# Performance work log

Hardware: AMD Instinct MI355X
Metric: run time of the kernel (lower is better)

The kernel has to match this reference:

```python
import jax, jax.numpy as jnp
import numpy as np

DN = ('NCDHW', 'OIDHW', 'NCDHW')

def conv(x, w, stride=1):
    k = w.shape[-1]
    pad = 'VALID' if k == 2 else 'SAME'  # ks=2,s=2 Minkowski offsets {0,1}; ks=3 centered; ks=1 pointwise
    return jax.lax.conv_general_dilated(x, w, (stride,) * 3, pad, dimension_numbers=DN)

def masked_bn(x, m, eps=1e-5):
    # BatchNorm over occupied voxels only (MinkowskiBatchNorm semantics); affine is identity at init.
    cnt = jnp.maximum(jnp.sum(m), 1.0)
    mean = jnp.sum(x * m, axis=(0, 2, 3, 4)) / cnt
    xc = (x - mean.reshape(1, -1, 1, 1, 1)) * m  # also zeroes unoccupied sites
    var = jnp.sum(xc * xc, axis=(0, 2, 3, 4)) / cnt
    return xc * jax.lax.rsqrt(var + eps).reshape(1, -1, 1, 1, 1)

def downmask(m):
    B, _, D, H, W = m.shape
    return m.reshape(B, 1, D // 2, 2, H // 2, 2, W // 2, 2).max(axis=(3, 5, 7))

def cbr(x, m, w):
    return jax.nn.relu(masked_bn(conv(x, w), m))

def res(x, m, wa, wb, wsk):
    y = masked_bn(conv(jax.nn.relu(masked_bn(conv(x, wa), m)), wb), m)
    sk = x if wsk is None else masked_bn(conv(x, wsk), m)
    return jax.nn.relu(y + sk)

def stage(x, m, wd, wa1, wb1, wsk, wa2, wb2):
    m2 = downmask(m)  # output coord set of ks=2,s=2 sparse conv
    x = jax.nn.relu(masked_bn(conv(x, wd, 2), m2))  # BasicConvolutionBlock
    x = res(x, m2, wa1, wb1, wsk)
    x = res(x, m2, wa2, wb2, None)
    return x, m2

def _forward(feats, mask, ws0, ws1, d1, a11, b11, a12, b12, d2, a21, b21, k2, a22, b22,
             d3, a31, b31, k3, a32, b32, d4, a41, b41, k4, a42, b42):
    m = mask
    x = cbr(feats * m, m, ws0)
    x = cbr(x, m, ws1)
    x, m = stage(x, m, d1, a11, b11, None, a12, b12)   # 32 -> 32 (identity skip)
    x, m = stage(x, m, d2, a21, b21, k2, a22, b22)     # 32 -> 64
    x, m = stage(x, m, d3, a31, b31, k3, a32, b32)     # 64 -> 128
    x, m = stage(x, m, d4, a41, b41, k4, a42, b42)     # 128 -> 256
    return x

def setup_inputs() -> dict:
    key = jax.random.key(0)
    ks = jax.random.split(key, 28)
    def W(k, o, i, s):
        return jax.random.normal(k, (o, i, s, s, s), jnp.float32) / np.sqrt(i * s ** 3)
    feats = jax.random.normal(ks[0], (2, 3, 64, 64, 64), jnp.float32)
    mask = (jax.random.uniform(ks[1], (2, 1, 64, 64, 64)) < 0.1).astype(jnp.float32)
    return dict(
        feats=feats * mask, mask=mask,
        ws0=W(ks[2], 32, 3, 3), ws1=W(ks[3], 32, 32, 3),
        d1=W(ks[4], 32, 32, 2), a11=W(ks[5], 32, 32, 3), b11=W(ks[6], 32, 32, 3),
        a12=W(ks[7], 32, 32, 3), b12=W(ks[8], 32, 32, 3),
        d2=W(ks[9], 32, 32, 2), a21=W(ks[10], 64, 32, 3), b21=W(ks[11], 64, 64, 3),
        k2=W(ks[12], 64, 32, 1), a22=W(ks[13], 64, 64, 3), b22=W(ks[14], 64, 64, 3),
        d3=W(ks[15], 64, 64, 2), a31=W(ks[16], 128, 64, 3), b31=W(ks[17], 128, 128, 3),
        k3=W(ks[18], 128, 64, 1), a32=W(ks[19], 128, 128, 3), b32=W(ks[20], 128, 128, 3),
        d4=W(ks[21], 128, 128, 2), a41=W(ks[22], 256, 128, 3), b41=W(ks[23], 256, 256, 3),
        k4=W(ks[24], 256, 128, 1), a42=W(ks[25], 256, 256, 3), b42=W(ks[26], 256, 256, 3))

def reference(feats, mask, ws0, ws1, d1, a11, b11, a12, b12, d2, a21, b21, k2, a22, b22,
              d3, a31, b31, k3, a32, b32, d4, a41, b41, k4, a42, b42):
    return _forward(feats, mask, ws0, ws1, d1, a11, b11, a12, b12, d2, a21, b21, k2, a22, b22,
                    d3, a31, b31, k3, a32, b32, d4, a41, b41, k4, a42, b42)
```

## Files before the change

### kernel.cpp

```cpp
#include <hip/hip_runtime.h>

#define BLK 256

static inline int gup(long work) { return (int)((work + BLK - 1) / BLK); }

__device__ inline bool occ_pred(const float* mask, const int* fmap,
                                int i, int DHW, int Ho, int Wo, int mode) {
  if (mode == 0) return mask[i] > 0.f;
  int b = i / DHW, sp = i - b * DHW;
  int HW = Ho * Wo;
  int z = sp / HW, r = sp - z * HW, y = r / Wo, x = r - y * Wo;
  int Hi = 2 * Ho, Wi = 2 * Wo;
  const int* mb = fmap + b * 8 * DHW;
  int base = ((2 * z) * Hi + 2 * y) * Wi + 2 * x;
  bool occ = false;
  for (int dz = 0; dz < 2; dz++)
    for (int dy = 0; dy < 2; dy++)
      for (int dx = 0; dx < 2; dx++)
        occ |= mb[base + dz * Hi * Wi + dy * Wi + dx] >= 0;
  return occ;
}

__global__ __launch_bounds__(1024) void cnt_k(const float* mask, const int* fmap,
    int* bcnt, int DHW, int Ho, int Wo, int mode, int total) {
  int i = blockIdx.x * 1024 + threadIdx.x;
  bool occ = (i < total) && occ_pred(mask, fmap, i, DHW, Ho, Wo, mode);
  unsigned long long bal = __ballot(occ);
  __shared__ int ws[16];
  int lane = threadIdx.x & 63, wid = threadIdx.x >> 6;
  if (lane == 0) ws[wid] = __popcll(bal);
  __syncthreads();
  if (threadIdx.x == 0) {
    int a = 0;
    for (int w = 0; w < 16; w++) a += ws[w];
    bcnt[blockIdx.x] = a;
  }
}

__global__ __launch_bounds__(1024) void scan_k(int* bcnt, int nb, int* cnt) {
  __shared__ int sh[1024];
  int t = threadIdx.x;
  int v = (t < nb) ? bcnt[t] : 0;
  sh[t] = v;
  __syncthreads();
  for (int o = 1; o < 1024; o <<= 1) {
    int u = (t >= o) ? sh[t - o] : 0;
    __syncthreads();
    sh[t] += u;
    __syncthreads();
  }
  if (t < nb) bcnt[t] = sh[t] - v;
  if (t == 0) *cnt = sh[1023];
}

__global__ __launch_bounds__(1024) void emit_k(const float* mask, const int* fmap,
    const int* boff, int* map, int* list, int DHW, int Ho, int Wo, int mode, int total) {
  int i = blockIdx.x * 1024 + threadIdx.x;
  bool occ = (i < total) && occ_pred(mask, fmap, i, DHW, Ho, Wo, mode);
  unsigned long long bal = __ballot(occ);
  int lane = threadIdx.x & 63, wid = threadIdx.x >> 6;
  __shared__ int wcnt[16], woff[16];
  if (lane == 0) wcnt[wid] = __popcll(bal);
  __syncthreads();
  if (threadIdx.x == 0) {
    int a = boff[blockIdx.x];
    for (int w = 0; w < 16; w++) { woff[w] = a; a += wcnt[w]; }
  }
  __syncthreads();
  if (i < total) {
    if (occ) {
      int p = woff[wid] + __popcll(bal & ((1ull << lane) - 1ull));
      map[i] = p; list[p] = i;
    } else map[i] = -1;
  }
}

__global__ __launch_bounds__(1024) void compact1_k(const int* __restrict__ fmap,
    int* __restrict__ map, int* __restrict__ list, int* __restrict__ cntp,
    int Do, int Ho, int Wo) {
  int DHW = Do * Ho * Wo, total = 2 * DHW;
  int tid = threadIdx.x, lane = tid & 63, wid = tid >> 6;
  bool occ = (tid < total) && occ_pred(nullptr, fmap, tid, DHW, Ho, Wo, 1);
  unsigned long long bal = __ballot(occ);
  __shared__ int wcnt[16], woff[16];
  if (lane == 0) wcnt[wid] = __popcll(bal);
  __syncthreads();
  if (tid == 0) {
    int a = 0;
    for (int w = 0; w < 16; w++) { woff[w] = a; a += wcnt[w]; }
    *cntp = a;
  }
  __syncthreads();
  if (tid < total) {
    if (occ) {
      int p = woff[wid] + __popcll(bal & ((1ull << lane) - 1ull));
      map[tid] = p; list[p] = tid;
    } else map[tid] = -1;
  }
}

__global__ __launch_bounds__(256) void csr_both_k(
    const int* __restrict__ list, const int* __restrict__ map,
    const int* __restrict__ cntp, const int* __restrict__ fmap,
    int* __restrict__ csr27, int* __restrict__ csr8,
    int D, int H, int W, int do8) {
  int n = *cntp;
  int DHW = D * H * W;
  for (int v = blockIdx.x * 256 + threadIdx.x; v < n; v += gridDim.x * 256) {
    int idx = list[v];
    int b = idx / DHW, sp = idx - b * DHW;
    int z = sp / (H * W), r = sp - z * H * W, y = r / W, x = r - y * W;
    const int* mb = map + b * DHW;
    int* e = csr27 + (long)v * 28;
    int cnt = 0;
    for (int k = 0; k < 27; k++) {
      int dz = k / 9 - 1, dy = (k / 3) % 3 - 1, dx = k % 3 - 1;
      int zz = z + dz, yy = y + dy, xx = x + dx;
      if ((unsigned)zz >= (unsigned)D || (unsigned)yy >= (unsigned)H ||
          (unsigned)xx >= (unsigned)W) continue;
      int j = mb[(zz * H + yy) * W + xx];
      if (j >= 0) e[++cnt] = (k << 24) | j;
    }
    e[0] = cnt;
    for (int s = cnt + 1; s <= 27; s++) e[s] = -1;
    if (do8) {
      int Hi = 2 * H, Wi = 2 * W;
      const int* fb = fmap + b * 8 * DHW;
      int* e8 = csr8 + (long)v * 9;
      int c8 = 0;
      for (int k = 0; k < 8; k++) {
        int dz = k >> 2, dy = (k >> 1) & 1, dx = k & 1;
        int j = fb[((2 * z + dz) * Hi + 2 * y + dy) * Wi + 2 * x + dx];
        if (j >= 0) e8[++c8] = (k << 24) | j;
      }
      e8[0] = c8;
      for (int s = c8 + 1; s <= 8; s++) e8[s] = -1;
    }
  }
}

struct WAll {
  const float* src[25];
  float* dst[25];
  int O[25], I[25], K[25];
  int sb[26];
};

__global__ __launch_bounds__(256) void wtr_all_k(WAll wa) {
  int b = blockIdx.x;
  int w = 0;
  while (w < 24 && b >= wa.sb[w + 1]) ++w;
  int O = wa.O[w], I = wa.I[w], K = wa.K[w];
  int I4 = (I + 3) >> 2;
  long tot = (long)K * I4 * O * 4;
  long t = (long)(b - wa.sb[w]) * 256 + threadIdx.x;
  if (t >= tot) return;
  int e = (int)(t & 3); long r = t >> 2;
  int co = (int)(r % O); long r2 = r / O;
  int ci4 = (int)(r2 % I4); int k = (int)(r2 / I4);
  int ci = 4 * ci4 + e;
  wa.dst[w][t] = (ci < I) ? wa.src[w][((long)co * I + ci) * K + k] : 0.f;
}

__global__ void gather0_k(const float* __restrict__ feats, const int* __restrict__ list,
                          const int* __restrict__ cntp, float* __restrict__ rows, int DHW) {
  int n = *cntp;
  int t = blockIdx.x * BLK + threadIdx.x;
  if (t >= n * 4) return;
  int vox = t >> 2, c = t & 3;
  int idx = list[vox]; int b = idx / DHW, sp = idx - b * DHW;
  rows[t] = (c < 3) ? feats[(b * 3 + c) * DHW + sp] : 0.f;
}

template <int CIN, int COUT, int CPT, int VX, int NT, bool PRE>
__global__ __launch_bounds__(256) void convk_k(
    const float* __restrict__ fin, const float* __restrict__ wt,
    float* __restrict__ fout, const int* __restrict__ csr,
    const int* __restrict__ cntp, const int* __restrict__ pcntp,
    const float* __restrict__ pslot, float* __restrict__ slot) {
  constexpr int CL = COUT / CPT;
  constexpr int G = 256 / CL;
  constexpr int VT = G * VX;
  constexpr int C4 = CIN / 4;
  constexpr int RST = C4 + 1;
  constexpr int WSZ = C4 * COUT;
  __shared__ int jtab[VT * NT];
  __shared__ float4 rbuf[VT * RST];
  __shared__ float4 wbuf[WSZ];
  __shared__ float aP[PRE ? CIN : 4], bP[PRE ? CIN : 4];
  __shared__ float swA[256], swB[256];
  int n = *cntp;
  int vb = blockIdx.x * VT;
  if (vb >= n) return;
  int tid = threadIdx.x;
  if constexpr (PRE) {
    int np = *pcntp;
    float c = fmaxf((float)np, 1.f);
    for (int ch = tid; ch < CIN; ch += 256) {
      float s = 0.f, q = 0.f;
      #pragma unroll
      for (int r = 0; r < 4; r++) { s += pslot[r * 512 + ch]; q += pslot[r * 512 + 256 + ch]; }
      float mean = s / c, var = fmaxf(q / c - mean * mean, 0.f);
      float a = rsqrtf(var + 1e-5f);
      aP[ch] = a; bP[ch] = -mean * a;
    }
  }
  for (int u = tid; u < VT * NT; u += 256) jtab[u] = -1;
  __syncthreads();
  for (int u = tid; u < VT * (NT + 1); u += 256) {
    int v = u / (NT + 1), s = u - v * (NT + 1);
    if (s > 0 && vb + v < n) {
      int e = csr[(long)(vb + v) * (NT + 1) + s];
      if (e >= 0) jtab[v * NT + (e >> 24)] = e & 0xFFFFFF;
    }
  }
  int cl = tid % CL, g = tid / CL, vg = g * VX;
  float acc[VX][CPT];
  #pragma unroll
  for (int vx = 0; vx < VX; vx++)
    #pragma unroll
    for (int m = 0; m < CPT; m++) acc[vx][m] = 0.f;
  const float4* fin4 = (const float4*)fin;
  const float4* w4 = (const float4*)wt;
  for (int k = 0; k < NT; k++) {
    __syncthreads();
    for (int u = tid; u < WSZ; u += 256) wbuf[u] = w4[(long)k * WSZ + u];
    for (int u = tid; u < VT * C4; u += 256) {
      int v = u / C4, c4 = u - v * C4;
      int j = jtab[v * NT + k];
      float4 val = make_float4(0.f, 0.f, 0.f, 0.f);
      if (j >= 0) {
        val = fin4[(long)j * C4 + c4];
        if constexpr (PRE) {
          int ch = 4 * c4;
          val.x = fmaxf(val.x * aP[ch] + bP[ch], 0.f);
          val.y = fmaxf(val.y * aP[ch + 1] + bP[ch + 1], 0.f);
          val.z = fmaxf(val.z * aP[ch + 2] + bP[ch + 2], 0.f);
          val.w = fmaxf(val.w * aP[ch + 3] + bP[ch + 3], 0.f);
        }
      }
      rbuf[v * RST + c4] = val;
    }
    __syncthreads();
    #pragma unroll
    for (int c4 = 0; c4 < C4; c4++) {
      float4 w_[CPT];
      #pragma unroll
      for (int m = 0; m < CPT; m++) w_[m] = wbuf[c4 * COUT + cl + m * CL];
      #pragma unroll
      for (int vx = 0; vx < VX; vx++) {
        float4 rv = rbuf[(vg + vx) * RST + c4];
        #pragma unroll
        for (int m = 0; m < CPT; m++)
          acc[vx][m] += rv.x * w_[m].x + rv.y * w_[m].y + rv.z * w_[m].z + rv.w * w_[m].w;
      }
    }
  }
  #pragma unroll
  for (int vx = 0; vx < VX; vx++) {
    int v = vb + vg + vx;
    if (v < n) {
      #pragma unroll
      for (int m = 0; m < CPT; m++)
        fout[(long)v * COUT + cl + m * CL] = acc[vx][m];
    }
  }
  int lane = tid & 63, wid = tid >> 6;
  #pragma unroll
  for (int m = 0; m < CPT; m++) {
    float ps = 0.f, pq = 0.f;
    #pragma unroll
    for (int vx = 0; vx < VX; vx++) { ps += acc[vx][m]; pq += acc[vx][m] * acc[vx][m]; }
    #pragma unroll
    for (int o = 32; o >= CL; o >>= 1) {
      ps += __shfl_down(ps, o);
      pq += __shfl_down(pq, o);
    }
    if (lane < CL) {
      swA[(m * 4 + wid) * CL + lane] = ps;
      swB[(m * 4 + wid) * CL + lane] = pq;
    }
  }
  __syncthreads();
  if (tid < COUT) {
    int m = tid / CL, c2 = tid % CL;
    float s = 0.f, q = 0.f;
    #pragma unroll
    for (int w = 0; w < 4; w++) {
      s += swA[(m * 4 + w) * CL + c2];
      q += swB[(m * 4 + w) * CL + c2];
    }
    float* sl = slot + (blockIdx.x & 3) * 512;
    atomicAdd(&sl[tid], s);
    atomicAdd(&sl[256 + tid], q);
  }
}

template <int CIN, int COUT, int COT, int VT, int KSP, bool PRE>
__global__ __launch_bounds__(256) void convw_k(
    const float* __restrict__ fin, const float* __restrict__ wt,
    float* __restrict__ fout, const int* __restrict__ csr,
    const int* __restrict__ cntp, const int* __restrict__ pcntp,
    const float* __restrict__ pslot) {
  constexpr int CL = COT / 2;
  constexpr int G = 256 / CL;
  constexpr int VX = VT / G;
  constexpr int C4 = CIN / 4;
  constexpr int RST = C4 + 1;
  __shared__ float4 wbuf[C4 * COT];
  __shared__ float4 rbuf[VT * RST];
  __shared__ int jt[VT * 27];
  __shared__ int act[27];
  __shared__ float aP[PRE ? CIN : 4], bP[PRE ? CIN : 4];
  int n = *cntp;
  int vb = blockIdx.x * VT;
  if (vb >= n) return;
  int tid = threadIdx.x;
  int c0 = blockIdx.y * COT;
  if constexpr (PRE) {
    int np = *pcntp;
    float c = fmaxf((float)np, 1.f);
    for (int ch = tid; ch < CIN; ch += 256) {
      float s = 0.f, q = 0.f;
      #pragma unroll
      for (int r = 0; r < 4; r++) { s += pslot[r * 512 + ch]; q += pslot[r * 512 + 256 + ch]; }
      float mean = s / c, var = fmaxf(q / c - mean * mean, 0.f);
      float a = rsqrtf(var + 1e-5f);
      aP[ch] = a; bP[ch] = -mean * a;
    }
  }
  if (tid < 27) act[tid] = 0;
  for (int u = tid; u < VT * 27; u += 256) jt[u] = -1;
  __syncthreads();
  for (int u = tid; u < VT * 28; u += 256) {
    int v = u / 28, s = u - v * 28;
    if (s > 0 && vb + v < n) {
      int e = csr[(long)(vb + v) * 28 + s];
      if (e >= 0) {
        int k = e >> 24;
        jt[v * 27 + k] = e & 0xFFFFFF;
        atomicOr(&act[k], 1);
      }
    }
  }
  __syncthreads();
  int cl = tid % CL, g = tid / CL, vg = g * VX;
  float acc[VX][2];
  #pragma unroll
  for (int vx = 0; vx < VX; vx++) { acc[vx][0] = 0.f; acc[vx][1] = 0.f; }
  const float4* fin4 = (const float4*)fin;
  const float4* w4 = (const float4*)wt;
  for (int k = blockIdx.z; k < 27; k += KSP) {
    if (!act[k]) continue;
    __syncthreads();
    for (int u = tid; u < C4 * COT; u += 256) {
      int ci4 = u / COT, co = u - ci4 * COT;
      wbuf[u] = w4[(long)k * C4 * COUT + ci4 * COUT + c0 + co];
    }
    for (int u = tid; u < VT * C4; u += 256) {
      int v = u / C4, c4 = u - v * C4;
      int j = jt[v * 27 + k];
      float4 val = make_float4(0.f, 0.f, 0.f, 0.f);
      if (j >= 0) {
        val = fin4[(long)j * C4 + c4];
        if constexpr (PRE) {
          int ch = 4 * c4;
          val.x = fmaxf(val.x * aP[ch] + bP[ch], 0.f);
          val.y = fmaxf(val.y * aP[ch + 1] + bP[ch + 1], 0.f);
          val.z = fmaxf(val.z * aP[ch + 2] + bP[ch + 2], 0.f);
          val.w = fmaxf(val.w * aP[ch + 3] + bP[ch + 3], 0.f);
        }
      }
      rbuf[v * RST + c4] = val;
    }
    __syncthreads();
    #pragma unroll 8
    for (int c4 = 0; c4 < C4; c4++) {
      float4 w0 = wbuf[c4 * COT + cl];
      float4 w1 = wbuf[c4 * COT + cl + CL];
      #pragma unroll
      for (int vx = 0; vx < VX; vx++) {
        float4 rv = rbuf[(vg + vx) * RST + c4];
        acc[vx][0] += rv.x * w0.x + rv.y * w0.y + rv.z * w0.z + rv.w * w0.w;
        acc[vx][1] += rv.x * w1.x + rv.y * w1.y + rv.z * w1.z + rv.w * w1.w;
      }
    }
  }
  #pragma unroll
  for (int vx = 0; vx < VX; vx++) {
    int v = vb + vg + vx;
    if (v < n) {
      atomicAdd(&fout[(long)v * COUT + c0 + cl], acc[vx][0]);
      atomicAdd(&fout[(long)v * COUT + c0 + cl + CL], acc[vx][1]);
    }
  }
}

template <int CIN, int COUT, int ES, bool PRE>
__global__ __launch_bounds__(256) void convc_k(
    const float* __restrict__ fin, const float* __restrict__ wt,
    float* __restrict__ fout, const int* __restrict__ csr,
    const int* __restrict__ cntp, const int* __restrict__ pcntp,
    const float* __restrict__ pslot, float* __restrict__ slot) {
  constexpr int CL = COUT / 2, G = 256 / CL, C4 = CIN / 4;
  constexpr int EST = (ES > 0) ? ES : 1;
  constexpr int CPD = PRE ? CIN : 4;
  __shared__ float4 rbuf[G * C4];
  __shared__ int se[G * EST];
  __shared__ float aP[CPD], bP[CPD];
  __shared__ float sA[256], sB[256];
  __shared__ int scmax;
  int n = *cntp;
  int vb = blockIdx.x * G;
  if (vb >= n) return;
  int tid = threadIdx.x;
  if constexpr (PRE) {
    int np = *pcntp;
    float c = fmaxf((float)np, 1.f);
    for (int ch = tid; ch < CIN; ch += 256) {
      float s = 0.f, q = 0.f;
      #pragma unroll
      for (int r = 0; r < 4; r++) { s += pslot[r * 512 + ch]; q += pslot[r * 512 + 256 + ch]; }
      float mean = s / c, var = fmaxf(q / c - mean * mean, 0.f);
      float a = rsqrtf(var + 1e-5f);
      aP[ch] = a; bP[ch] = -mean * a;
    }
  }
  int cmax;
  if constexpr (ES > 0) {
    if (tid == 0) scmax = 0;
    __syncthreads();
    for (int u = tid; u < G * ES; u += 256) {
      int v = vb + u / ES;
      int e = (v < n) ? csr[(long)vb * ES + u] : 0;
      se[u] = e;
      if ((u % ES) == 0) atomicMax(&scmax, e);
    }
    __syncthreads();
    cmax = scmax;
  } else {
    __syncthreads();
    cmax = 1;
  }
  int cl = tid % CL, g = tid / CL;
  int v = vb + g;
  bool alive = v < n;
  float a0 = 0.f, a1 = 0.f;
  const float4* fin4 = (const float4*)fin;
  const float4* w4 = (const float4*)wt;
  for (int i = 1; i <= cmax; i++) {
    __syncthreads();
    for (int u = tid; u < G * C4; u += 256) {
      int gg = u / C4, c4 = u - gg * C4;
      int pj = -1;
      if constexpr (ES > 0) {
        if (vb + gg < n && i <= se[gg * EST]) pj = se[gg * EST + i];
      } else {
        if (vb + gg < n) pj = vb + gg;
      }
      float4 val = make_float4(0.f, 0.f, 0.f, 0.f);
      if (pj >= 0) {
        int j = pj & 0xFFFFFF;
        val = fin4[(long)j * C4 + c4];
        if constexpr (PRE) {
          int ch = 4 * c4;
          val.x = fmaxf(val.x * aP[ch] + bP[ch], 0.f);
          val.y = fmaxf(val.y * aP[ch + 1] + bP[ch + 1], 0.f);
          val.z = fmaxf(val.z * aP[ch + 2] + bP[ch + 2], 0.f);
          val.w = fmaxf(val.w * aP[ch + 3] + bP[ch + 3], 0.f);
        }
      }
      rbuf[u] = val;
    }
    __syncthreads();
    int pj;
    if constexpr (ES > 0) {
      pj = (alive && i <= se[g * EST]) ? se[g * EST + i] : -1;
    } else {
      pj = alive ? v : -1;
    }
    if (pj >= 0) {
      int k = pj >> 24;
      const float4* wk = w4 + (long)k * C4 * COUT + cl;
      #pragma unroll 8
      for (int c4 = 0; c4 < C4; c4++) {
        float4 rv = rbuf[g * C4 + c4];
        float4 w0 = wk[c4 * COUT];
        float4 w1 = wk[c4 * COUT + CL];
        a0 += rv.x * w0.x + rv.y * w0.y + rv.z * w0.z + rv.w * w0.w;
        a1 += rv.x * w1.x + rv.y * w1.y + rv.z * w1.z + rv.w * w1.w;
      }
    }
  }
  if (alive) {
    fout[(long)v * COUT + cl] = a0;
    fout[(long)v * COUT + cl + CL] = a1;
  }
  __syncthreads();
  sA[tid] = alive ? a0 : 0.f; sB[tid] = alive ? a1 : 0.f;
  __syncthreads();
  for (int o = 128; o >= CL; o >>= 1) {
    if (tid < o) { sA[tid] += sA[tid + o]; sB[tid] += sB[tid + o]; }
    __syncthreads();
  }
  float s0 = 0.f, s1 = 0.f;
  if (tid < CL) { s0 = sA[tid]; s1 = sB[tid]; }
  __syncthreads();
  sA[tid] = alive ? a0 * a0 : 0.f; sB[tid] = alive ? a1 * a1 : 0.f;
  __syncthreads();
  for (int o = 128; o >= CL; o >>= 1) {
    if (tid < o) { sA[tid] += sA[tid + o]; sB[tid] += sB[tid + o]; }
    __syncthreads();
  }
  if (tid < CL) {
    float* sl = slot + (blockIdx.x & 3) * 512;
    atomicAdd(&sl[tid], s0);
    atomicAdd(&sl[tid + CL], s1);
    atomicAdd(&sl[256 + tid], sA[tid]);
    atomicAdd(&sl[256 + tid + CL], sB[tid]);
  }
}

template <int C>
__global__ __launch_bounds__(BLK) void bnred_k(const float* __restrict__ rows,
    const int* __restrict__ cntp, float* __restrict__ slot) {
  int n = *cntp;
  long tot = (long)n * C;
  int tid = threadIdx.x;
  float s = 0.f, s2 = 0.f;
  for (long t = (long)blockIdx.x * BLK + tid; t < tot; t += (long)gridDim.x * BLK) {
    float v = rows[t]; s += v; s2 += v * v;
  }
  __shared__ float sh[BLK], sh2[BLK];
  sh[tid] = s; sh2[tid] = s2;
  __syncthreads();
  for (int o = BLK / 2; o >= C; o >>= 1) {
    if (tid < o) { sh[tid] += sh[tid + o]; sh2[tid] += sh2[tid + o]; }
    __syncthreads();
  }
  if (tid < C) { atomicAdd(&slot[tid], sh[tid]); atomicAdd(&slot[256 + tid], sh2[tid]); }
}

template <int C, int MODE>
__global__ __launch_bounds__(256) void skipapp_k(
    const float* __restrict__ x, const float* __restrict__ y,
    const float* __restrict__ s1, const float* __restrict__ s2,
    const int* __restrict__ cntp, float* __restrict__ out) {
  __shared__ float a1_[C], b1_[C], a2_[C], b2_[C];
  int n = *cntp;
  int tid = threadIdx.x;
  float cnt = fmaxf((float)n, 1.f);
  for (int c = tid; c < C; c += 256) {
    float s = 0.f, q = 0.f;
    #pragma unroll
    for (int r = 0; r < 4; r++) { s += s1[r * 512 + c]; q += s1[r * 512 + 256 + c]; }
    float mean = s / cnt, var = fmaxf(q / cnt - mean * mean, 0.f);
    float a = rsqrtf(var + 1e-5f);
    a1_[c] = a; b1_[c] = -mean * a;
    if (MODE != 2) {
      s = 0.f; q = 0.f;
      #pragma unroll
      for (int r = 0; r < 4; r++) { s += s2[r * 512 + c]; q += s2[r * 512 + 256 + c]; }
      mean = s / cnt; var = fmaxf(q / cnt - mean * mean, 0.f);
      a = rsqrtf(var + 1e-5f);
      a2_[c] = a; b2_[c] = -mean * a;
    }
  }
  __syncthreads();
  constexpr int C4 = C / 4;
  long tot = (long)n * C4;
  for (long t = (long)blockIdx.x * 256 + tid; t < tot; t += (long)gridDim.x * 256) {
    int c = 4 * (int)(t % C4);
    float4 xv = ((const float4*)x)[t];
    float4 yv = ((const float4*)y)[t];
    float4 o;
    o.x = xv.x * a1_[c] + b1_[c];
    o.y = xv.y * a1_[c + 1] + b1_[c + 1];
    o.z = xv.z * a1_[c + 2] + b1_[c + 2];
    o.w = xv.w * a1_[c + 3] + b1_[c + 3];
    if (MODE == 0) {
      o.x += yv.x * a2_[c] + b2_[c];
      o.y += yv.y * a2_[c + 1] + b2_[c + 1];
      o.z += yv.z * a2_[c + 2] + b2_[c + 2];
      o.w += yv.w * a2_[c + 3] + b2_[c + 3];
    } else if (MODE == 1) {
      o.x += fmaxf(yv.x * a2_[c] + b2_[c], 0.f);
      o.y += fmaxf(yv.y * a2_[c + 1] + b2_[c + 1], 0.f);
      o.z += fmaxf(yv.z * a2_[c + 2] + b2_[c + 2], 0.f);
      o.w += fmaxf(yv.w * a2_[c + 3] + b2_[c + 3], 0.f);
    } else {
      o.x += yv.x; o.y += yv.y; o.z += yv.z; o.w += yv.w;
    }
    o.x = fmaxf(o.x, 0.f); o.y = fmaxf(o.y, 0.f);
    o.z = fmaxf(o.z, 0.f); o.w = fmaxf(o.w, 0.f);
    ((float4*)out)[t] = o;
  }
}

__global__ void scatter_k(const float* __restrict__ rows, const int* __restrict__ list,
                          const int* __restrict__ cntp, float* __restrict__ out, int DHW) {
  int n = *cntp;
  int t = blockIdx.x * BLK + threadIdx.x;
  if (t >= n * 256) return;
  int vox = t >> 8, c = t & 255;
  int idx = list[vox]; int b = idx / DHW, sp = idx - b * DHW;
  out[(b * 256 + c) * DHW + sp] = rows[t];
}

#define CAP0 81920
#define CAP1 57344
#define CAP2 8192
#define CAP3 1024
#define CAP4 128

extern "C" void kernel_launch(void* const* d_in, const int* in_sizes, int n_in,
                              void* d_out, int out_size, void* d_ws, size_t ws_size,
                              hipStream_t stream) {
  const float* feats = (const float*)d_in[0];
  const float* mask0 = (const float*)d_in[1];

  char* p = (char*)d_ws;
  auto alloc = [&](size_t bytes) { char* r = p; p += (bytes + 255) & ~255ull; return r; };

  const int tab[25][4] = {
    {2, 32, 3, 27},  {3, 32, 32, 27}, {4, 32, 32, 8},  {5, 32, 32, 27}, {6, 32, 32, 27},
    {7, 32, 32, 27}, {8, 32, 32, 27}, {9, 32, 32, 8},  {10, 64, 32, 27},{11, 64, 64, 27},
    {12, 64, 32, 1}, {13, 64, 64, 27},{14, 64, 64, 27},{15, 64, 64, 8}, {16, 128, 64, 27},
    {17, 128, 128, 27},{18, 128, 64, 1},{19, 128, 128, 27},{20, 128, 128, 27},
    {21, 128, 128, 8},{22, 256, 128, 27},{23, 256, 256, 27},{24, 256, 128, 1},
    {25, 256, 256, 27},{26, 256, 256, 27},
  };
  WAll wa;
  float* wT[27] = {nullptr};
  int blk = 0;
  for (int i = 0; i < 25; i++) {
    int idx = tab[i][0], O = tab[i][1], I = tab[i][2], K = tab[i][3];
    int I4 = (I + 3) / 4;
    long sz = (long)K * I4 * O * 4;
    wT[idx] = (float*)alloc((size_t)sz * 4);
    wa.src[i] = (const float*)d_in[idx]; wa.dst[i] = wT[idx];
    wa.O[i] = O; wa.I[i] = I; wa.K[i] = K;
    wa.sb[i] = blk; blk += (int)((sz + 255) / 256);
  }
  wa.sb[25] = blk;

  int* map0 = (int*)alloc(524288 * 4);
  int* list0 = (int*)alloc((size_t)CAP0 * 4);
  int* map1 = (int*)alloc(65536 * 4);
  int* list1 = (int*)alloc((size_t)CAP1 * 4);
  int* map2 = (int*)alloc(8192 * 4);
  int* list2 = (int*)alloc(8192 * 4);
  int* map3 = (int*)alloc(1024 * 4);
  int* list3 = (int*)alloc(1024 * 4);
  int* map4 = (int*)alloc(128 * 4);
  int* list4 = (int*)alloc(128 * 4);
  int* bcnt = (int*)alloc(1024 * 4);
  int* cnts = (int*)alloc(32 * 4);
  int* c27_0 = (int*)alloc((size_t)CAP0 * 28 * 4);
  int* c27_1 = (int*)alloc((size_t)CAP1 * 28 * 4);
  int* c8_1  = (int*)alloc((size_t)CAP1 * 9 * 4);
  int* c27_2 = (int*)alloc((size_t)CAP2 * 28 * 4);
  int* c8_2  = (int*)alloc((size_t)CAP2 * 9 * 4);
  int* c27_3 = (int*)alloc((size_t)CAP3 * 28 * 4);
  int* c8_3  = (int*)alloc((size_t)CAP3 * 9 * 4);
  int* c27_4 = (int*)alloc((size_t)CAP4 * 28 * 4);
  int* c8_4  = (int*)alloc((size_t)CAP4 * 9 * 4);
  float* stats = (float*)alloc(25 * 2048 * 4);
  float* G0  = (float*)alloc((size_t)CAP0 * 4 * 4);
  float* F0a = (float*)alloc((size_t)CAP0 * 32 * 4);
  float* F0b = (float*)alloc((size_t)CAP0 * 32 * 4);
  float *R1[4], *R2[4];
  for (int i = 0; i < 4; i++) R1[i] = (float*)alloc((size_t)CAP1 * 32 * 4);
  for (int i = 0; i < 4; i++) R2[i] = (float*)alloc((size_t)CAP2 * 64 * 4);
  size_t z3sz = (size_t)CAP3 * 128 * 4 * 6 + (size_t)CAP4 * 256 * 4 * 6;
  float* Z3 = (float*)alloc(z3sz);
  float* R3[6], *R4[6];
  for (int i = 0; i < 6; i++) R3[i] = Z3 + (size_t)i * CAP3 * 128;
  for (int i = 0; i < 6; i++) R4[i] = Z3 + (size_t)6 * CAP3 * 128 + (size_t)i * CAP4 * 256;

  hipMemsetAsync(stats, 0, 25 * 2048 * 4, stream);
  hipMemsetAsync(Z3, 0, z3sz, stream);
  hipMemsetAsync(d_out, 0, (size_t)out_size * 4, stream);

  wtr_all_k<<<blk, 256, 0, stream>>>(wa);

  int* n0 = cnts + 0; int* n1 = cnts + 1; int* n2 = cnts + 2;
  int* n3 = cnts + 3; int* n4 = cnts + 4;

  cnt_k<<<512, 1024, 0, stream>>>(mask0, nullptr, bcnt, 262144, 64, 64, 0, 524288);
  scan_k<<<1, 1024, 0, stream>>>(bcnt, 512, n0);
  emit_k<<<512, 1024, 0, stream>>>(mask0, nullptr, bcnt, map0, list0, 262144, 64, 64, 0, 524288);
  gather0_k<<<gup((long)CAP0 * 4), BLK, 0, stream>>>(feats, list0, n0, G0, 262144);
  csr_both_k<<<512, 256, 0, stream>>>(list0, map0, n0, nullptr, c27_0, nullptr, 64, 64, 64, 0);

  cnt_k<<<64, 1024, 0, stream>>>(nullptr, map0, bcnt, 32768, 32, 32, 1, 65536);
  scan_k<<<1, 1024, 0, stream>>>(bcnt, 64, n1);
  emit_k<<<64, 1024, 0, stream>>>(nullptr, map0, bcnt, map1, list1, 32768, 32, 32, 1, 65536);
  csr_both_k<<<256, 256, 0, stream>>>(list1, map1, n1, map0, c27_1, c8_1, 32, 32, 32, 1);

  cnt_k<<<8, 1024, 0, stream>>>(nullptr, map1, bcnt, 4096, 16, 16, 1, 8192);
  scan_k<<<1, 1024, 0, stream>>>(bcnt, 8, n2);
  emit_k<<<8, 1024, 0, stream>>>(nullptr, map1, bcnt, map2, list2, 4096, 16, 16, 1, 8192);
  csr_both_k<<<32, 256, 0, stream>>>(list2, map2, n2, map1, c27_2, c8_2, 16, 16, 16, 1);

  compact1_k<<<1, 1024, 0, stream>>>(map2, map3, list3, n3, 8, 8, 8);
  csr_both_k<<<4, 256, 0, stream>>>(list3, map3, n3, map2, c27_3, c8_3, 8, 8, 8, 1);

  compact1_k<<<1, 1024, 0, stream>>>(map3, map4, list4, n4, 4, 4, 4);
  csr_both_k<<<1, 256, 0, stream>>>(list4, map4, n4, map3, c27_4, c8_4, 4, 4, 4, 1);

  auto slot = [&](int i) { return stats + (size_t)i * 2048; };
  auto bgrid = [&](long cap, int C) { long g = (cap * C / 4 + 255) / 256; return (int)(g > 2048 ? 2048 : g); };

  {
    int g = (CAP0 + 63) / 64;
    convk_k<4, 32, 4, 2, 27, false><<<g, 256, 0, stream>>>(G0, wT[2], F0a, c27_0, n0, nullptr, nullptr, slot(0));
    convk_k<32, 32, 4, 2, 27, true><<<g, 256, 0, stream>>>(F0a, wT[3], F0b, c27_0, n0, n0, slot(0), slot(1));
  }

  {
    int g = (CAP1 + 63) / 64, ag = bgrid(CAP1, 32);
    convk_k<32, 32, 4, 2, 8, true><<<g, 256, 0, stream>>>(F0b, wT[4], R1[0], c8_1, n1, n0, slot(1), slot(2));
    convk_k<32, 32, 4, 2, 27, true><<<g, 256, 0, stream>>>(R1[0], wT[5], R1[1], c27_1, n1, n1, slot(2), slot(3));
    convk_k<32, 32, 4, 2, 27, true><<<g, 256, 0, stream>>>(R1[1], wT[6], R1[2], c27_1, n1, n1, slot(3), slot(4));
    skipapp_k<32, 1><<<ag, 256, 0, stream>>>(R1[2], R1[0], slot(4), slot(2), n1, R1[3]);
    convk_k<32, 32, 4, 2, 27, false><<<g, 256, 0, stream>>>(R1[3], wT[7], R1[1], c27_1, n1, nullptr, nullptr, slot(5));
    convk_k<32, 32, 4, 2, 27, true><<<g, 256, 0, stream>>>(R1[1], wT[8], R1[2], c27_1, n1, n1, slot(5), slot(6));
    skipapp_k<32, 2><<<ag, 256, 0, stream>>>(R1[2], R1[3], slot(6), nullptr, n1, R1[0]);
  }

  {
    int g32 = (CAP2 + 31) / 32, ag = bgrid(CAP2, 64);
    convk_k<32, 32, 4, 1, 8, false><<<g32, 256, 0, stream>>>(R1[0], wT[9], R2[0], c8_2, n2, nullptr, nullptr, slot(7));
    convk_k<32, 64, 4, 2, 27, true><<<g32, 256, 0, stream>>>(R2[0], wT[10], R2[1], c27_2, n2, n2, slot(7), slot(8));
    convk_k<64, 64, 4, 2, 27, true><<<g32, 256, 0, stream>>>(R2[1], wT[11], R2[2], c27_2, n2, n2, slot(8), slot(9));
    convc_k<32, 64, 0, true><<<(CAP2 + 7) / 8, 256, 0, stream>>>(R2[0], wT[12], R2[3], nullptr, n2, n2, slot(7), slot(10));
    skipapp_k<64, 0><<<ag, 256, 0, stream>>>(R2[2], R2[3], slot(9), slot(10), n2, R2[1]);
    convk_k<64, 64, 4, 2, 27, false><<<g32, 256, 0, stream>>>(R2[1], wT[13], R2[0], c27_2, n2, nullptr, nullptr, slot(11));
    convk_k<64, 64, 4, 2, 27, true><<<g32, 256, 0, stream>>>(R2[0], wT[14], R2[2], c27_2, n2, n2, slot(11), slot(12));
    skipapp_k<64, 2><<<ag, 256, 0, stream>>>(R2[2], R2[1], slot(12), nullptr, n2, R2[3]);
  }

  {
    int gP = (CAP3 + 7) / 8, gO = (CAP3 + 3) / 4, ag = bgrid(CAP3, 128);
    int rO = gup((long)CAP3 * 128); if (rO > 512) rO = 512;
    dim3 gw(CAP3 / 16, 1, 4);
    convc_k<64, 64, 9, false><<<gP, 256, 0, stream>>>(R2[3], wT[15], R3[0], c8_3, n3, nullptr, nullptr, slot(13));
    convw_k<64, 128, 128, 16, 4, true><<<gw, 256, 0, stream>>>(R3[0], wT[16], R3[1], c27_3, n3, n3, slot(13));
    bnred_k<128><<<rO, BLK, 0, stream>>>(R3[1], n3, slot(14));
    convw_k<128, 128, 128, 16, 4, true><<<gw, 256, 0, stream>>>(R3[1], wT[17], R3[2], c27_3, n3, n3, slot(14));
    bnred_k<128><<<rO, BLK, 0, stream>>>(R3[2], n3, slot(15));
    convc_k<64, 128, 0, true><<<gO, 256, 0, stream>>>(R3[0], wT[18], R3[3], nullptr, n3, n3, slot(13), slot(16));
    skipapp_k<128, 0><<<ag, 256, 0, stream>>>(R3[2], R3[3], slot(15), slot(16), n3, R3[1]);
    convw_k<128, 128, 128, 16, 4, false><<<gw, 256, 0, stream>>>(R3[1], wT[19], R3[4], c27_3, n3, nullptr, nullptr);
    bnred_k<128><<<rO, BLK, 0, stream>>>(R3[4], n3, slot(17));
    convw_k<128, 128, 128, 16, 4, true><<<gw, 256, 0, stream>>>(R3[4], wT[20], R3[5], c27_3, n3, n3, slot(17));
    bnred_k<128><<<rO, BLK, 0, stream>>>(R3[5], n3, slot(18));
    skipapp_k<128, 2><<<ag, 256, 0, stream>>>(R3[5], R3[1], slot(18), nullptr, n3, R3[0]);
  }

  {
    int gP = (CAP4 + 3) / 4, gO = (CAP4 + 1) / 2, ag = bgrid(CAP4, 256);
    int rO = gup((long)CAP4 * 256); if (rO > 512) rO = 512;
    dim3 gw(CAP4 / 16, 4, 8);
    convc_k<128, 128, 9, false><<<gP, 256, 0, stream>>>(R3[0], wT[21], R4[0], c8_4, n4, nullptr, nullptr, slot(19));
    convw_k<128, 256, 64, 16, 8, true><<<gw, 256, 0, stream>>>(R4[0], wT[22], R4[1], c27_4, n4, n4, slot(19));
    bnred_k<256><<<rO, BLK, 0, stream>>>(R4[1], n4, slot(20));
    convw_k<256, 256, 64, 16, 8, true><<<gw, 256, 0, stream>>>(R4[1], wT[23], R4[2], c27_4, n4, n4, slot(20));
    bnred_k<256><<<rO, BLK, 0, stream>>>(R4[2], n4, slot(21));
    convc_k<128, 256, 0, true><<<gO, 256, 0, stream>>>(R4[0], wT[24], R4[3], nullptr, n4, n4, slot(19), slot(22));
    skipapp_k<256, 0><<<ag, 256, 0, stream>>>(R4[2], R4[3], slot(21), slot(22), n4, R4[1]);
    convw_k<256, 256, 64, 16, 8, false><<<gw, 256, 0, stream>>>(R4[1], wT[25], R4[4], c27_4, n4, nullptr, nullptr);
    bnred_k<256><<<rO, BLK, 0, stream>>>(R4[4], n4, slot(23));
    convw_k<256, 256, 64, 16, 8, true><<<gw, 256, 0, stream>>>(R4[4], wT[26], R4[5], c27_4, n4, n4, slot(23));
    bnred_k<256><<<rO, BLK, 0, stream>>>(R4[5], n4, slot(24));
    skipapp_k<256, 2><<<ag, 256, 0, stream>>>(R4[5], R4[1], slot(24), nullptr, n4, R4[0]);
  }

  scatter_k<<<gup((long)CAP4 * 256), BLK, 0, stream>>>(R4[0], list4, n4, (float*)d_out, 64);
}
```

Measured before the change: 1.498 ms.

## Split kernel offsets across grid y with atomic accumulation and separate BN reduction

The convk_k gather convolutions in stages 0-2 now split the 27 (or 8) kernel offsets across blockIdx.y and accumulate partial outputs into pre-zeroed buffers with atomicAdd. Because partial sums no longer give final per-block statistics, BN statistics are computed by separate bnred_k passes, and the buffers are zeroed by a new memset. It also raises voxels per thread and interleaves voxel assignment across thread groups. The aim is more parallelism and occupancy for the small early stages, at the cost of extra atomics, memsets and reduction kernels, plus nondeterministic summation order.

Measured after the change: 1.649 ms. +10.1%, slower.

```diff
diff --git a/kernel.cpp b/kernel.cpp
--- a/kernel.cpp
+++ b/kernel.cpp
@@ -172,7 +172,7 @@
   rows[t] = (c < 3) ? feats[(b * 3 + c) * DHW + sp] : 0.f;
 }
 
-template <int CIN, int COUT, int CPT, int VX, int NT, bool PRE>
+template <int CIN, int COUT, int CPT, int VX, int NT, int TG, bool PRE>
 __global__ __launch_bounds__(256) void convk_k(
     const float* __restrict__ fin, const float* __restrict__ wt,
     float* __restrict__ fout, const int* __restrict__ csr,
@@ -214,7 +214,7 @@
       if (e >= 0) jtab[v * NT + (e >> 24)] = e & 0xFFFFFF;
     }
   }
-  int cl = tid % CL, g = tid / CL, vg = g * VX;
+  int cl = tid % CL, g = tid / CL;
   float acc[VX][CPT];
   #pragma unroll
   for (int vx = 0; vx < VX; vx++)
@@ -222,7 +222,8 @@
     for (int m = 0; m < CPT; m++) acc[vx][m] = 0.f;
   const float4* fin4 = (const float4*)fin;
   const float4* w4 = (const float4*)wt;
-  for (int k = 0; k < NT; k++) {
+  const int tg0 = (TG > 1) ? (int)blockIdx.y : 0;
+  for (int k = tg0; k < NT; k += TG) {
     __syncthreads();
     for (int u = tid; u < WSZ; u += 256) wbuf[u] = w4[(long)k * WSZ + u];
     for (int u = tid; u < VT * C4; u += 256) {
@@ -249,7 +250,7 @@
       for (int m = 0; m < CPT; m++) w_[m] = wbuf[c4 * COUT + cl + m * CL];
       #pragma unroll
       for (int vx = 0; vx < VX; vx++) {
-        float4 rv = rbuf[(vg + vx) * RST + c4];
+        float4 rv = rbuf[(g + vx * G) * RST + c4];
         #pragma unroll
         for (int m = 0; m < CPT; m++)
           acc[vx][m] += rv.x * w_[m].x + rv.y * w_[m].y + rv.z * w_[m].z + rv.w * w_[m].w;
@@ -258,41 +259,51 @@
   }
   #pragma unroll
   for (int vx = 0; vx < VX; vx++) {
-    int v = vb + vg + vx;
+    int v = vb + g + vx * G;
     if (v < n) {
       #pragma unroll
-      for (int m = 0; m < CPT; m++)
-        fout[(long)v * COUT + cl + m * CL] = acc[vx][m];
-    }
-  }
-  int lane = tid & 63, wid = tid >> 6;
-  #pragma unroll
-  for (int m = 0; m < CPT; m++) {
-    float ps = 0.f, pq = 0.f;
+      for (int m = 0; m < CPT; m++) {
+        if constexpr (TG > 1)
+          atomicAdd(&fout[(long)v * COUT + cl + m * CL], acc[vx][m]);
+        else
+          fout[(long)v * COUT + cl + m * CL] = acc[vx][m];
+      }
+    }
+  }
+  if constexpr (TG == 1) {
+    int lane = tid & 63, wid = tid >> 6;
+    bool alive[VX];
     #pragma unroll
-    for (int vx = 0; vx < VX; vx++) { ps += acc[vx][m]; pq += acc[vx][m] * acc[vx][m]; }
+    for (int vx = 0; vx < VX; vx++) alive[vx] = (vb + g + vx * G) < n;
     #pragma unroll
-    for (int o = 32; o >= CL; o >>= 1) {
-      ps += __shfl_down(ps, o);
-      pq += __shfl_down(pq, o);
-    }
-    if (lane < CL) {
-      swA[(m * 4 + wid) * CL + lane] = ps;
-      swB[(m * 4 + wid) * CL + lane] = pq;
-    }
-  }
-  __syncthreads();
-  if (tid < COUT) {
-    int m = tid / CL, c2 = tid % CL;
-    float s = 0.f, q = 0.f;
-    #pragma unroll
-    for (int w = 0; w < 4; w++) {
-      s += swA[(m * 4 + w) * CL + c2];
-      q += swB[(m * 4 + w) * CL + c2];
-    }
-    float* sl = slot + (blockIdx.x & 3) * 512;
-    atomicAdd(&sl[tid], s);
-    atomicAdd(&sl[256 + tid], q);
+    for (int m = 0; m < CPT; m++) {
+      float ps = 0.f, pq = 0.f;
+      #pragma unroll
+      for (int vx = 0; vx < VX; vx++)
+        if (alive[vx]) { ps += acc[vx][m]; pq += acc[vx][m] * acc[vx][m]; }
+      #pragma unroll
+      for (int o = 32; o >= CL; o >>= 1) {
+        ps += __shfl_down(ps, o);
+        pq += __shfl_down(pq, o);
+      }
+      if (lane < CL) {
+        swA[(m * 4 + wid) * CL + lane] = ps;
+        swB[(m * 4 + wid) * CL + lane] = pq;
+      }
+    }
+    __syncthreads();
+    if (tid < COUT) {
+      int m = tid / CL, c2 = tid % CL;
+      float s = 0.f, q = 0.f;
+      #pragma unroll
+      for (int w = 0; w < 4; w++) {
+        s += swA[(m * 4 + w) * CL + c2];
+        q += swB[(m * 4 + w) * CL + c2];
+      }
+      float* sl = slot + (blockIdx.x & 3) * 512;
+      atomicAdd(&sl[tid], s);
+      atomicAdd(&sl[256 + tid], q);
+    }
   }
 }
 
@@ -668,10 +679,13 @@
   float* stats = (float*)alloc(25 * 2048 * 4);
   float* G0  = (float*)alloc((size_t)CAP0 * 4 * 4);
   float* F0a = (float*)alloc((size_t)CAP0 * 32 * 4);
+  char* zstart = p;
   float* F0b = (float*)alloc((size_t)CAP0 * 32 * 4);
-  float *R1[4], *R2[4];
-  for (int i = 0; i < 4; i++) R1[i] = (float*)alloc((size_t)CAP1 * 32 * 4);
-  for (int i = 0; i < 4; i++) R2[i] = (float*)alloc((size_t)CAP2 * 64 * 4);
+  float* R1[6];
+  for (int i = 0; i < 6; i++) R1[i] = (float*)alloc((size_t)CAP1 * 32 * 4);
+  float* R2[6];
+  for (int i = 0; i < 6; i++) R2[i] = (float*)alloc((size_t)CAP2 * 64 * 4);
+  size_t zlen = (size_t)(p - zstart);
   size_t z3sz = (size_t)CAP3 * 128 * 4 * 6 + (size_t)CAP4 * 256 * 4 * 6;
   float* Z3 = (float*)alloc(z3sz);
   float* R3[6], *R4[6];
@@ -679,6 +693,7 @@
   for (int i = 0; i < 6; i++) R4[i] = Z3 + (size_t)6 * CAP3 * 128 + (size_t)i * CAP4 * 256;
 
   hipMemsetAsync(stats, 0, 25 * 2048 * 4, stream);
+  hipMemsetAsync(zstart, 0, zlen, stream);
   hipMemsetAsync(Z3, 0, z3sz, stream);
   hipMemsetAsync(d_out, 0, (size_t)out_size * 4, stream);
 
@@ -712,33 +727,46 @@
   auto slot = [&](int i) { return stats + (size_t)i * 2048; };
   auto bgrid = [&](long cap, int C) { long g = (cap * C / 4 + 255) / 256; return (int)(g > 2048 ? 2048 : g); };
 
+  int rb0 = 512, rb1 = 512, rb2 = 512;
+
   {
-    int g = (CAP0 + 63) / 64;
-    convk_k<4, 32, 4, 2, 27, false><<<g, 256, 0, stream>>>(G0, wT[2], F0a, c27_0, n0, nullptr, nullptr, slot(0));
-    convk_k<32, 32, 4, 2, 27, true><<<g, 256, 0, stream>>>(F0a, wT[3], F0b, c27_0, n0, n0, slot(0), slot(1));
+    int g = CAP0 / 128;
+    convk_k<4, 32, 4, 4, 27, 1, false><<<g, 256, 0, stream>>>(G0, wT[2], F0a, c27_0, n0, nullptr, nullptr, slot(0));
+    convk_k<32, 32, 4, 4, 27, 2, true><<<dim3(g, 2), 256, 0, stream>>>(F0a, wT[3], F0b, c27_0, n0, n0, slot(0), nullptr);
+    bnred_k<32><<<rb0, BLK, 0, stream>>>(F0b, n0, slot(1));
   }
 
   {
-    int g = (CAP1 + 63) / 64, ag = bgrid(CAP1, 32);
-    convk_k<32, 32, 4, 2, 8, true><<<g, 256, 0, stream>>>(F0b, wT[4], R1[0], c8_1, n1, n0, slot(1), slot(2));
-    convk_k<32, 32, 4, 2, 27, true><<<g, 256, 0, stream>>>(R1[0], wT[5], R1[1], c27_1, n1, n1, slot(2), slot(3));
-    convk_k<32, 32, 4, 2, 27, true><<<g, 256, 0, stream>>>(R1[1], wT[6], R1[2], c27_1, n1, n1, slot(3), slot(4));
+    int g = CAP1 / 128, ag = bgrid(CAP1, 32);
+    convk_k<32, 32, 4, 4, 8, 2, true><<<dim3(g, 2), 256, 0, stream>>>(F0b, wT[4], R1[0], c8_1, n1, n0, slot(1), nullptr);
+    bnred_k<32><<<rb1, BLK, 0, stream>>>(R1[0], n1, slot(2));
+    convk_k<32, 32, 4, 4, 27, 2, true><<<dim3(g, 2), 256, 0, stream>>>(R1[0], wT[5], R1[1], c27_1, n1, n1, slot(2), nullptr);
+    bnred_k<32><<<rb1, BLK, 0, stream>>>(R1[1], n1, slot(3));
+    convk_k<32, 32, 4, 4, 27, 2, true><<<dim3(g, 2), 256, 0, stream>>>(R1[1], wT[6], R1[2], c27_1, n1, n1, slot(3), nullptr);
+    bnred_k<32><<<rb1, BLK, 0, stream>>>(R1[2], n1, slot(4));
     skipapp_k<32, 1><<<ag, 256, 0, stream>>>(R1[2], R1[0], slot(4), slot(2), n1, R1[3]);
-    convk_k<32, 32, 4, 2, 27, false><<<g, 256, 0, stream>>>(R1[3], wT[7], R1[1], c27_1, n1, nullptr, nullptr, slot(5));
-    convk_k<32, 32, 4, 2, 27, true><<<g, 256, 0, stream>>>(R1[1], wT[8], R1[2], c27_1, n1, n1, slot(5), slot(6));
-    skipapp_k<32, 2><<<ag, 256, 0, stream>>>(R1[2], R1[3], slot(6), nullptr, n1, R1[0]);
+    convk_k<32, 32, 4, 4, 27, 2, false><<<dim3(g, 2), 256, 0, stream>>>(R1[3], wT[7], R1[4], c27_1, n1, nullptr, nullptr, nullptr);
+    bnred_k<32><<<rb1, BLK, 0, stream>>>(R1[4], n1, slot(5));
+    convk_k<32, 32, 4, 4, 27, 2, true><<<dim3(g, 2), 256, 0, stream>>>(R1[4], wT[8], R1[5], c27_1, n1, n1, slot(5), nullptr);
+    bnred_k<32><<<rb1, BLK, 0, stream>>>(R1[5], n1, slot(6));
+    skipapp_k<32, 2><<<ag, 256, 0, stream>>>(R1[5], R1[3], slot(6), nullptr, n1, R1[3]);
   }
 
   {
-    int g32 = (CAP2 + 31) / 32, ag = bgrid(CAP2, 64);
-    convk_k<32, 32, 4, 1, 8, false><<<g32, 256, 0, stream>>>(R1[0], wT[9], R2[0], c8_2, n2, nullptr, nullptr, slot(7));
-    convk_k<32, 64, 4, 2, 27, true><<<g32, 256, 0, stream>>>(R2[0], wT[10], R2[1], c27_2, n2, n2, slot(7), slot(8));
-    convk_k<64, 64, 4, 2, 27, true><<<g32, 256, 0, stream>>>(R2[1], wT[11], R2[2], c27_2, n2, n2, slot(8), slot(9));
+    int g64 = CAP2 / 64, ag = bgrid(CAP2, 64);
+    convk_k<32, 32, 4, 2, 8, 2, false><<<dim3(g64 * 2, 2), 256, 0, stream>>>(R1[3], wT[9], R2[0], c8_2, n2, nullptr, nullptr, nullptr);
+    bnred_k<32><<<rb2, BLK, 0, stream>>>(R2[0], n2, slot(7));
+    convk_k<32, 64, 4, 4, 27, 4, true><<<dim3(g64, 4), 256, 0, stream>>>(R2[0], wT[10], R2[1], c27_2, n2, n2, slot(7), nullptr);
+    bnred_k<64><<<rb2, BLK, 0, stream>>>(R2[1], n2, slot(8));
+    convk_k<64, 64, 4, 4, 27, 4, true><<<dim3(g64, 4), 256, 0, stream>>>(R2[1], wT[11], R2[2], c27_2, n2, n2, slot(8), nullptr);
+    bnred_k<64><<<rb2, BLK, 0, stream>>>(R2[2], n2, slot(9));
     convc_k<32, 64, 0, true><<<(CAP2 + 7) / 8, 256, 0, stream>>>(R2[0], wT[12], R2[3], nullptr, n2, n2, slot(7), slot(10));
-    skipapp_k<64, 0><<<ag, 256, 0, stream>>>(R2[2], R2[3], slot(9), slot(10), n2, R2[1]);
-    convk_k<64, 64, 4, 2, 27, false><<<g32, 256, 0, stream>>>(R2[1], wT[13], R2[0], c27_2, n2, nullptr, nullptr, slot(11));
-    convk_k<64, 64, 4, 2, 27, true><<<g32, 256, 0, stream>>>(R2[0], wT[14], R2[2], c27_2, n2, n2, slot(11), slot(12));
-    skipapp_k<64, 2><<<ag, 256, 0, stream>>>(R2[2], R2[1], slot(12), nullptr, n2, R2[3]);
+    skipapp_k<64, 0><<<ag, 256, 0, stream>>>(R2[2], R2[3], slot(9), slot(10), n2, R2[3]);
+    convk_k<64, 64, 4, 4, 27, 4, false><<<dim3(g64, 4), 256, 0, stream>>>(R2[3], wT[13], R2[4], c27_2, n2, nullptr, nullptr, nullptr);
+    bnred_k<64><<<rb2, BLK, 0, stream>>>(R2[4], n2, slot(11));
+    convk_k<64, 64, 4, 4, 27, 4, true><<<dim3(g64, 4), 256, 0, stream>>>(R2[4], wT[14], R2[5], c27_2, n2, n2, slot(11), nullptr);
+    bnred_k<64><<<rb2, BLK, 0, stream>>>(R2[5], n2, slot(12));
+    skipapp_k<64, 2><<<ag, 256, 0, stream>>>(R2[5], R2[3], slot(12), nullptr, n2, R2[3]);
   }
 
   {
```

## Double-buffer conv tap loads through registers to overlap gathers with FMA

Applied to the files above, without the earlier changes.

The sparse conv kernel now prefetches the next kernel tap's weights and gathered input rows into registers while computing the current tap. It then writes them into a second LDS buffer, which removes one barrier per tap. This doubles shared memory use and adds register pressure, which may reduce occupancy for large channel configurations. It also adds a guard so that voxels past the end are excluded from the BN statistics.

Result: slower. 1.612 ms (+7.6%).

```diff
diff --git a/kernel.cpp b/kernel.cpp
--- a/kernel.cpp
+++ b/kernel.cpp
@@ -184,9 +184,11 @@
   constexpr int C4 = CIN / 4;
   constexpr int RST = C4 + 1;
   constexpr int WSZ = C4 * COUT;
+  constexpr int NRS = (VT * C4 + 255) / 256;
+  constexpr int NWS = (WSZ + 255) / 256;
   __shared__ int jtab[VT * NT];
-  __shared__ float4 rbuf[VT * RST];
-  __shared__ float4 wbuf[WSZ];
+  __shared__ float4 rbuf[2][VT * RST];
+  __shared__ float4 wbuf[2][WSZ];
   __shared__ float aP[PRE ? CIN : 4], bP[PRE ? CIN : 4];
   __shared__ float swA[256], swB[256];
   int n = *cntp;
@@ -214,47 +216,84 @@
       if (e >= 0) jtab[v * NT + (e >> 24)] = e & 0xFFFFFF;
     }
   }
+  __syncthreads();
+  const float4* fin4 = (const float4*)fin;
+  const float4* w4 = (const float4*)wt;
+
+  float4 rreg[NRS], wreg[NWS];
+  int jr[NRS];
+  auto stage_regs = [&](int k) {
+    #pragma unroll
+    for (int s = 0; s < NWS; s++) {
+      int u = tid + s * 256;
+      if (u < WSZ) wreg[s] = w4[(long)k * WSZ + u];
+    }
+    #pragma unroll
+    for (int s = 0; s < NRS; s++) {
+      int u = tid + s * 256;
+      jr[s] = -1;
+      if (u < VT * C4) {
+        int v = u / C4, c4 = u - v * C4;
+        int j = jtab[v * NT + k];
+        jr[s] = j;
+        if (j >= 0) rreg[s] = fin4[(long)j * C4 + c4];
+      }
+    }
+  };
+  auto write_lds = [&](int b) {
+    #pragma unroll
+    for (int s = 0; s < NWS; s++) {
+      int u = tid + s * 256;
+      if (u < WSZ) wbuf[b][u] = wreg[s];
+    }
+    #pragma unroll
+    for (int s = 0; s < NRS; s++) {
+      int u = tid + s * 256;
+      if (u < VT * C4) {
+        int v = u / C4, c4 = u - v * C4;
+        float4 val = make_float4(0.f, 0.f, 0.f, 0.f);
+        if (jr[s] >= 0) {
+          val = rreg[s];
+          if constexpr (PRE) {
+            int ch = 4 * c4;
+            val.x = fmaxf(val.x * aP[ch] + bP[ch], 0.f);
+            val.y = fmaxf(val.y * aP[ch + 1] + bP[ch + 1], 0.f);
+            val.z = fmaxf(val.z * aP[ch + 2] + bP[ch + 2], 0.f);
+            val.w = fmaxf(val.w * aP[ch + 3] + bP[ch + 3], 0.f);
+          }
+        }
+        rbuf[b][v * RST + c4] = val;
+      }
+    }
+  };
+
   int cl = tid % CL, g = tid / CL, vg = g * VX;
   float acc[VX][CPT];
   #pragma unroll
   for (int vx = 0; vx < VX; vx++)
     #pragma unroll
     for (int m = 0; m < CPT; m++) acc[vx][m] = 0.f;
-  const float4* fin4 = (const float4*)fin;
-  const float4* w4 = (const float4*)wt;
+
+  stage_regs(0);
+  write_lds(0);
   for (int k = 0; k < NT; k++) {
     __syncthreads();
-    for (int u = tid; u < WSZ; u += 256) wbuf[u] = w4[(long)k * WSZ + u];
-    for (int u = tid; u < VT * C4; u += 256) {
-      int v = u / C4, c4 = u - v * C4;
-      int j = jtab[v * NT + k];
-      float4 val = make_float4(0.f, 0.f, 0.f, 0.f);
-      if (j >= 0) {
-        val = fin4[(long)j * C4 + c4];
-        if constexpr (PRE) {
-          int ch = 4 * c4;
-          val.x = fmaxf(val.x * aP[ch] + bP[ch], 0.f);
-          val.y = fmaxf(val.y * aP[ch + 1] + bP[ch + 1], 0.f);
-          val.z = fmaxf(val.z * aP[ch + 2] + bP[ch + 2], 0.f);
-          val.w = fmaxf(val.w * aP[ch + 3] + bP[ch + 3], 0.f);
-        }
-      }
-      rbuf[v * RST + c4] = val;
-    }
-    __syncthreads();
+    if (k + 1 < NT) stage_regs(k + 1);
+    int b = k & 1;
     #pragma unroll
     for (int c4 = 0; c4 < C4; c4++) {
       float4 w_[CPT];
       #pragma unroll
-      for (int m = 0; m < CPT; m++) w_[m] = wbuf[c4 * COUT + cl + m * CL];
+      for (int m = 0; m < CPT; m++) w_[m] = wbuf[b][c4 * COUT + cl + m * CL];
       #pragma unroll
       for (int vx = 0; vx < VX; vx++) {
-        float4 rv = rbuf[(vg + vx) * RST + c4];
+        float4 rv = rbuf[b][(vg + vx) * RST + c4];
         #pragma unroll
         for (int m = 0; m < CPT; m++)
           acc[vx][m] += rv.x * w_[m].x + rv.y * w_[m].y + rv.z * w_[m].z + rv.w * w_[m].w;
       }
     }
+    if (k + 1 < NT) write_lds((k + 1) & 1);
   }
   #pragma unroll
   for (int vx = 0; vx < VX; vx++) {
@@ -270,7 +309,9 @@
   for (int m = 0; m < CPT; m++) {
     float ps = 0.f, pq = 0.f;
     #pragma unroll
-    for (int vx = 0; vx < VX; vx++) { ps += acc[vx][m]; pq += acc[vx][m] * acc[vx][m]; }
+    for (int vx = 0; vx < VX; vx++) {
+      if (vb + vg + vx < n) { ps += acc[vx][m]; pq += acc[vx][m] * acc[vx][m]; }
+    }
     #pragma unroll
     for (int o = 32; o >= CL; o >>= 1) {
       ps += __shfl_down(ps, o);
```
